# Optimization experiments

Hardware: AMD Instinct MI355X
Metric: run time of the kernel (lower is better)

The kernel has to match this reference:

```python
import jax, jax.numpy as jnp
import numpy as np

B, T, D, HEADS = 4, 2048, 2048, 16  # math requires T == D


def setup_inputs() -> dict:
    key = jax.random.key(0)
    k1, k2, k3 = jax.random.split(key, 3)
    scale = 1.0 / np.sqrt(D)
    x = jax.random.normal(k1, (B, T, D), dtype=jnp.float32)
    w_qk = jax.random.normal(k2, (2 * D, D), dtype=jnp.float32) * scale
    w_dense = jax.random.normal(k3, (D, D), dtype=jnp.float32) * scale
    b_dense = jnp.zeros((D,), dtype=jnp.float32)
    return {"x": x, "w_qk": w_qk, "w_dense": w_dense, "b_dense": b_dense}


def reference(x, w_qk, w_dense, b_dense):
    b, t, d = x.shape
    h = HEADS
    vh = d // h
    # to_q_k: Linear(d, 2d, bias=False); chunk into k0, v
    kv = jnp.einsum('btd,ed->bte', x, w_qk)          # [b,t,2d]
    k0, v = kv[..., :d], kv[..., d:]                 # each [b,t,d]
    scale_factor = 1.0 / jnp.sqrt(jnp.asarray(d * (d - 1) / 2, dtype=x.dtype))
    # k = k0.transpose(1,2) -> [b,d,t]; scores = k @ v^T -> [b,d,t] (t==d)
    s = jnp.einsum('bmi,bjm->bij', k0, v) * scale_factor   # [b,d,t]
    a = jax.nn.softmax(s, axis=-1)
    q = jnp.einsum('bit,btd->bid', a, v)             # [b,d,d]
    # q.transpose(0,1).chunk(h, dim=0) -> stack(dim=1) -> transpose(1,2) -> reshape
    qt = jnp.swapaxes(q, 0, 1)                       # [d, b, d]
    stk = qt.reshape(h, vh, b, d)                    # h chunks of [vh,b,d]
    stk = jnp.transpose(stk, (1, 0, 2, 3))           # stack(dim=1): [vh,h,b,d]
    stk = jnp.transpose(stk, (0, 2, 1, 3))           # transpose(1,2): [vh,b,h,d]
    out = stk.reshape(b, t, d)
    # dropout in eval mode == identity; to_dense Linear
    return jnp.einsum('btd,ed->bte', out, w_dense) + b_dense
```

## Files before the change

### kernel.cpp

```cpp
#include <hip/hip_runtime.h>
#include <stdint.h>
#include <math.h>


typedef __bf16 bf16x8 __attribute__((ext_vector_type(8)));
typedef float  f32x4  __attribute__((ext_vector_type(4)));

__device__ __forceinline__ float bf2f(uint16_t u) {
  union { uint32_t i; float f; } c; c.i = ((uint32_t)u) << 16; return c.f;
}
__device__ __forceinline__ uint16_t f2bf(float f) {
  union { float f; uint32_t i; } c; c.f = f;
  uint32_t i = c.i;
  return (uint16_t)((i + 0x7fffu + ((i >> 16) & 1u)) >> 16);
}

#define NX4 4194304u
#define NW4 2097152u
#define ND4 1048576u
__global__ __launch_bounds__(256) void k_cast_all(
    const float* __restrict__ x, const float* __restrict__ wqk,
    const float* __restrict__ wd, uint16_t* __restrict__ dst) {
  uint32_t i = blockIdx.x * 256 + threadIdx.x;
  float4 v;
  if (i < NX4)            v = reinterpret_cast<const float4*>(x)[i];
  else if (i < NX4 + NW4) v = reinterpret_cast<const float4*>(wqk)[i - NX4];
  else                    v = reinterpret_cast<const float4*>(wd)[i - NX4 - NW4];
  ushort4 o;
  o.x = f2bf(v.x); o.y = f2bf(v.y); o.z = f2bf(v.z); o.w = f2bf(v.w);
  reinterpret_cast<ushort4*>(dst)[i] = o;
}

__device__ __forceinline__ const uint16_t* stage_ptr(
    const uint16_t* base, int tile_row0, int c, int lda) {
  const int tid = threadIdx.x;
  const int r3 = tid >> 3;
  const int ko = (((tid & 7) ^ (r3 & 7)) * 8);
  return base + (size_t)(tile_row0 + c * 32 + r3) * lda + ko;
}

__device__ __forceinline__ void gemm_core_reg(
    const uint16_t* a0, const uint16_t* a1, const uint16_t* a2, const uint16_t* a3,
    const uint16_t* b0, const uint16_t* b1, const uint16_t* b2, const uint16_t* b3,
    uint16_t* As, uint16_t* Bs, int K, f32x4 acc[4][4])
{
  const int tid = threadIdx.x;
  const int w = tid >> 6, l = tid & 63;
  const int wm = (w >> 1) * 64, wn = (w & 1) * 64;
  const int frow = l & 15, fkc = l >> 4;
  const int xr = frow & 7;
  const int off0 = (fkc ^ xr) * 8;
  const int off1 = ((4 + fkc) ^ xr) * 8;
  const int lw = (tid >> 3) * 64 + (tid & 7) * 8;

  uint4 ra0, ra1, ra2, ra3, rb0, rb1, rb2, rb3;
  ra0 = *reinterpret_cast<const uint4*>(a0); a0 += 64;
  ra1 = *reinterpret_cast<const uint4*>(a1); a1 += 64;
  ra2 = *reinterpret_cast<const uint4*>(a2); a2 += 64;
  ra3 = *reinterpret_cast<const uint4*>(a3); a3 += 64;
  rb0 = *reinterpret_cast<const uint4*>(b0); b0 += 64;
  rb1 = *reinterpret_cast<const uint4*>(b1); b1 += 64;
  rb2 = *reinterpret_cast<const uint4*>(b2); b2 += 64;
  rb3 = *reinterpret_cast<const uint4*>(b3); b3 += 64;

  for (int kb = 0; kb < K; kb += 64) {
    __syncthreads();
    *reinterpret_cast<uint4*>(&As[lw])        = ra0;
    *reinterpret_cast<uint4*>(&As[lw + 2048]) = ra1;
    *reinterpret_cast<uint4*>(&As[lw + 4096]) = ra2;
    *reinterpret_cast<uint4*>(&As[lw + 6144]) = ra3;
    *reinterpret_cast<uint4*>(&Bs[lw])        = rb0;
    *reinterpret_cast<uint4*>(&Bs[lw + 2048]) = rb1;
    *reinterpret_cast<uint4*>(&Bs[lw + 4096]) = rb2;
    *reinterpret_cast<uint4*>(&Bs[lw + 6144]) = rb3;
    __syncthreads();
    if (kb + 64 < K) {
      ra0 = *reinterpret_cast<const uint4*>(a0); a0 += 64;
      ra1 = *reinterpret_cast<const uint4*>(a1); a1 += 64;
      ra2 = *reinterpret_cast<const uint4*>(a2); a2 += 64;
      ra3 = *reinterpret_cast<const uint4*>(a3); a3 += 64;
      rb0 = *reinterpret_cast<const uint4*>(b0); b0 += 64;
      rb1 = *reinterpret_cast<const uint4*>(b1); b1 += 64;
      rb2 = *reinterpret_cast<const uint4*>(b2); b2 += 64;
      rb3 = *reinterpret_cast<const uint4*>(b3); b3 += 64;
    }
#pragma unroll
    for (int h = 0; h < 2; ++h) {
      const int off = h ? off1 : off0;
      bf16x8 af[4], bfv[4];
#pragma unroll
      for (int mi = 0; mi < 4; ++mi)
        af[mi] = *reinterpret_cast<const bf16x8*>(&As[(wm + mi * 16 + frow) * 64 + off]);
#pragma unroll
      for (int ni = 0; ni < 4; ++ni)
        bfv[ni] = *reinterpret_cast<const bf16x8*>(&Bs[(wn + ni * 16 + frow) * 64 + off]);
#pragma unroll
      for (int mi = 0; mi < 4; ++mi)
#pragma unroll
        for (int ni = 0; ni < 4; ++ni)
          acc[mi][ni] = __builtin_amdgcn_mfma_f32_16x16x32_bf16(af[mi], bfv[ni], acc[mi][ni], 0, 0, 0);
    }
  }
}

__global__ __launch_bounds__(256) void k_gemm_kv(
    const uint16_t* __restrict__ W,
    const uint16_t* __restrict__ X,
    uint16_t* __restrict__ k0T,
    uint16_t* __restrict__ vT)
{
  __shared__ uint16_t As[8192], Bs[8192];
  const int bm = blockIdx.y, bn = blockIdx.x;
  f32x4 acc[4][4];
#pragma unroll
  for (int i = 0; i < 4; ++i)
#pragma unroll
    for (int j = 0; j < 4; ++j) acc[i][j] = (f32x4){0.f, 0.f, 0.f, 0.f};
  gemm_core_reg(stage_ptr(W, bm * 128, 0, 2048), stage_ptr(W, bm * 128, 1, 2048),
                stage_ptr(W, bm * 128, 2, 2048), stage_ptr(W, bm * 128, 3, 2048),
                stage_ptr(X, bn * 128, 0, 2048), stage_ptr(X, bn * 128, 1, 2048),
                stage_ptr(X, bn * 128, 2, 2048), stage_ptr(X, bn * 128, 3, 2048),
                As, Bs, 2048, acc);
  const int tid = threadIdx.x;
  const int w = tid >> 6, l = tid & 63;
  const int wm = (w >> 1) * 64, wn = (w & 1) * 64;
  const int cr = (l >> 4) * 4, cc = l & 15;
  uint16_t* Cb = (bm < 16) ? (k0T + (size_t)bm * 128 * 8192)
                           : (vT + (size_t)(bm - 16) * 128 * 8192);
#pragma unroll
  for (int mi = 0; mi < 4; ++mi)
#pragma unroll
    for (int ni = 0; ni < 4; ++ni)
#pragma unroll
      for (int g = 0; g < 4; ++g) {
        int lr = wm + mi * 16 + cr + g;
        int bt = bn * 128 + wn + ni * 16 + cc;
        Cb[(size_t)lr * 8192 + bt] = f2bf(acc[mi][ni][g]);
      }
}

__global__ __launch_bounds__(256) void k_gemm_bt(
    const uint16_t* __restrict__ A, int lda, long sA,
    const uint16_t* __restrict__ B, int ldb, long sB,
    uint16_t* __restrict__ C, int ldc, long sC,
    int K, float scale)
{
  __shared__ uint16_t As[8192], Bs[8192];
  const int z = blockIdx.z;
  A += (size_t)z * sA; B += (size_t)z * sB; C += (size_t)z * sC;
  const int bm = blockIdx.y, bn = blockIdx.x;
  f32x4 acc[4][4];
#pragma unroll
  for (int i = 0; i < 4; ++i)
#pragma unroll
    for (int j = 0; j < 4; ++j) acc[i][j] = (f32x4){0.f, 0.f, 0.f, 0.f};
  gemm_core_reg(stage_ptr(A, bm * 128, 0, lda), stage_ptr(A, bm * 128, 1, lda),
                stage_ptr(A, bm * 128, 2, lda), stage_ptr(A, bm * 128, 3, lda),
                stage_ptr(B, bn * 128, 0, ldb), stage_ptr(B, bn * 128, 1, ldb),
                stage_ptr(B, bn * 128, 2, ldb), stage_ptr(B, bn * 128, 3, ldb),
                As, Bs, K, acc);
  const int tid = threadIdx.x;
  const int w = tid >> 6, l = tid & 63;
  const int wm = (w >> 1) * 64, wn = (w & 1) * 64;
  const int cr = (l >> 4) * 4, cc = l & 15;
#pragma unroll
  for (int mi = 0; mi < 4; ++mi)
#pragma unroll
    for (int ni = 0; ni < 4; ++ni)
#pragma unroll
      for (int g = 0; g < 4; ++g) {
        int grow = bm * 128 + wm + mi * 16 + cr + g;
        int gcol = bn * 128 + wn + ni * 16 + cc;
        C[(size_t)grow * ldc + gcol] = f2bf(acc[mi][ni][g] * scale);
      }
}

__device__ __forceinline__ size_t qrow_off(int rr) {
  int bp = rr >> 11, tp = rr & 2047;
  int bi = (tp >> 4) & 3;
  int i  = (tp & 15) * 128 + bp * 32 + (tp >> 6);
  return ((size_t)bi * 2048 + (size_t)i) * 2048;
}

__global__ __launch_bounds__(256) void k_gemm_out(
    const uint16_t* __restrict__ Q,
    const uint16_t* __restrict__ W,
    const float*    __restrict__ bias,
    float*          __restrict__ Out)
{
  __shared__ uint16_t As[8192], Bs[8192];
  const int tid = threadIdx.x;
  const int bm = blockIdx.y, bn = blockIdx.x;
  const int r3 = tid >> 3;
  const int ko = ((tid & 7) ^ (r3 & 7)) * 8;
  const uint16_t* a0 = Q + qrow_off(bm * 128 + 0 * 32 + r3) + ko;
  const uint16_t* a1 = Q + qrow_off(bm * 128 + 1 * 32 + r3) + ko;
  const uint16_t* a2 = Q + qrow_off(bm * 128 + 2 * 32 + r3) + ko;
  const uint16_t* a3 = Q + qrow_off(bm * 128 + 3 * 32 + r3) + ko;
  f32x4 acc[4][4];
#pragma unroll
  for (int i = 0; i < 4; ++i)
#pragma unroll
    for (int j = 0; j < 4; ++j) acc[i][j] = (f32x4){0.f, 0.f, 0.f, 0.f};
  gemm_core_reg(a0, a1, a2, a3,
                stage_ptr(W, bn * 128, 0, 2048), stage_ptr(W, bn * 128, 1, 2048),
                stage_ptr(W, bn * 128, 2, 2048), stage_ptr(W, bn * 128, 3, 2048),
                As, Bs, 2048, acc);
  const int w = tid >> 6, l = tid & 63;
  const int wm = (w >> 1) * 64, wn = (w & 1) * 64;
  const int cr = (l >> 4) * 4, cc = l & 15;
#pragma unroll
  for (int mi = 0; mi < 4; ++mi)
#pragma unroll
    for (int ni = 0; ni < 4; ++ni)
#pragma unroll
      for (int g = 0; g < 4; ++g) {
        int grow = bm * 128 + wm + mi * 16 + cr + g;
        int gcol = bn * 128 + wn + ni * 16 + cc;
        Out[(size_t)grow * 2048 + gcol] = acc[mi][ni][g] + bias[gcol];
      }
}

__global__ __launch_bounds__(256) void k_transpose(
    const uint16_t* __restrict__ src, uint16_t* __restrict__ dst)
{
  __shared__ uint16_t tile[64][65];
  const int tid = threadIdx.x;
  const int bx = blockIdx.x;
  const int by = blockIdx.y;
  const int cu = tid & 31, r0 = tid >> 5;
#pragma unroll
  for (int p = 0; p < 8; ++p) {
    int r = p * 8 + r0;
    uint32_t v = *reinterpret_cast<const uint32_t*>(
        &src[(size_t)(by * 64 + r) * 8192 + bx * 64 + cu * 2]);
    tile[r][cu * 2]     = (uint16_t)(v & 0xffffu);
    tile[r][cu * 2 + 1] = (uint16_t)(v >> 16);
  }
  __syncthreads();
#pragma unroll
  for (int p = 0; p < 8; ++p) {
    int r = p * 8 + r0;
    uint32_t lo = tile[cu * 2][r], hi = tile[cu * 2 + 1][r];
    *reinterpret_cast<uint32_t*>(
        &dst[(size_t)(bx * 64 + r) * 2048 + by * 64 + cu * 2]) = lo | (hi << 16);
  }
}

__global__ __launch_bounds__(256) void k_softmax(uint16_t* __restrict__ s)
{
  uint16_t* p = s + (size_t)blockIdx.x * 2048;
  const int tid = threadIdx.x;
  uint4 raw = reinterpret_cast<const uint4*>(p)[tid];
  uint32_t u[4] = {raw.x, raw.y, raw.z, raw.w};
  float x[8];
#pragma unroll
  for (int i = 0; i < 4; ++i) {
    x[2 * i]     = bf2f((uint16_t)(u[i] & 0xffffu));
    x[2 * i + 1] = bf2f((uint16_t)(u[i] >> 16));
  }
  float m = x[0];
#pragma unroll
  for (int i = 1; i < 8; ++i) m = fmaxf(m, x[i]);
#pragma unroll
  for (int o = 32; o; o >>= 1) m = fmaxf(m, __shfl_xor(m, o, 64));
  __shared__ float redm[4], reds[4];
  if ((tid & 63) == 0) redm[tid >> 6] = m;
  __syncthreads();
  m = fmaxf(fmaxf(redm[0], redm[1]), fmaxf(redm[2], redm[3]));
  float sum = 0.f;
#pragma unroll
  for (int i = 0; i < 8; ++i) { x[i] = __expf(x[i] - m); sum += x[i]; }
#pragma unroll
  for (int o = 32; o; o >>= 1) sum += __shfl_xor(sum, o, 64);
  if ((tid & 63) == 0) reds[tid >> 6] = sum;
  __syncthreads();
  sum = reds[0] + reds[1] + reds[2] + reds[3];
  float inv = 1.0f / sum;
  uint32_t ou[4];
#pragma unroll
  for (int i = 0; i < 4; ++i) {
    uint32_t lo = f2bf(x[2 * i] * inv);
    uint32_t hi = f2bf(x[2 * i + 1] * inv);
    ou[i] = lo | (hi << 16);
  }
  reinterpret_cast<uint4*>(p)[tid] = make_uint4(ou[0], ou[1], ou[2], ou[3]);
}

extern "C" void kernel_launch(void* const* d_in, const int* in_sizes, int n_in,
                              void* d_out, int out_size, void* d_ws, size_t ws_size,
                              hipStream_t stream) {
  const float* x       = (const float*)d_in[0];
  const float* w_qk    = (const float*)d_in[1];
  const float* w_dense = (const float*)d_in[2];
  const float* b_dense = (const float*)d_in[3];
  float* out = (float*)d_out;

  const size_t NX = 4ull * 2048 * 2048;
  const size_t NW = 4096ull * 2048;
  const size_t ND = 2048ull * 2048;

  uint16_t* xb   = (uint16_t*)d_ws;
  uint16_t* wqkb = xb + NX;
  uint16_t* wdb  = wqkb + NW;
  uint16_t* k0T  = wdb + ND;
  uint16_t* vT   = k0T + NX;
  uint16_t* qb   = xb;
  uint16_t* Vn   = (uint16_t*)d_out;
  uint16_t* sb   = Vn + NX;

  const float scale = (float)(1.0 / sqrt(0.5 * 2048.0 * 2047.0));

  k_cast_all<<<dim3((NX4 + NW4 + ND4) / 256), 256, 0, stream>>>(x, w_qk, w_dense, xb);

  k_gemm_kv<<<dim3(64, 32), 256, 0, stream>>>(wqkb, xb, k0T, vT);
  k_transpose<<<dim3(128, 32), 256, 0, stream>>>(vT, Vn);
  k_gemm_bt<<<dim3(16, 16, 4), 256, 0, stream>>>(
      k0T, 8192, 2048L, Vn, 2048, 2048L * 2048L, sb, 2048, 2048L * 2048L, 2048, scale);
  k_softmax<<<dim3(8192), 256, 0, stream>>>(sb);
  k_gemm_bt<<<dim3(16, 16, 4), 256, 0, stream>>>(
      sb, 2048, 2048L * 2048L, vT, 8192, 2048L, qb, 2048, 2048L * 2048L, 2048, 1.0f);
  k_gemm_out<<<dim3(16, 64), 256, 0, stream>>>(qb, wdb, b_dense, out);
}
```

Before: 536.2 us.

## Rewrite GEMM core with 256x256 tiles, direct global-to-LDS loads and double buffering

All four GEMMs now share a new core that uses 256x256 block tiles with 512 threads, 128 KiB of dynamic LDS, and global_load_lds to stream tiles straight into LDS. Loads are double-buffered, with explicit vmcnt waits and barriers, and MFMA bursts run at raised wave priority. The goal is more data reuse per block and overlap of memory traffic with MFMA work, removing the register round-trip staging of the old loop. In exchange, the grids become much smaller (256 blocks for the batched GEMMs), which can leave CUs underused, and the hand-written wait counts must be exactly right to stay correct.

```diff
diff --git a/kernel.cpp b/kernel.cpp
--- a/kernel.cpp
+++ b/kernel.cpp
@@ -5,6 +5,9 @@
 
 typedef __bf16 bf16x8 __attribute__((ext_vector_type(8)));
 typedef float  f32x4  __attribute__((ext_vector_type(4)));
+
+typedef __attribute__((address_space(3))) uint32_t lds_u32_t;
+typedef __attribute__((address_space(1))) const uint32_t glb_u32_t;
 
 __device__ __forceinline__ float bf2f(uint16_t u) {
   union { uint32_t i; float f; } c; c.i = ((uint32_t)u) << 16; return c.f;
@@ -14,6 +17,14 @@
   uint32_t i = c.i;
   return (uint16_t)((i + 0x7fffu + ((i >> 16) & 1u)) >> 16);
 }
+
+__device__ __forceinline__ void glds16(const uint16_t* g, const char* l) {
+  __builtin_amdgcn_global_load_lds((glb_u32_t*)g, (lds_u32_t*)l, 16, 0, 0);
+}
+
+#define FENCE() asm volatile("" ::: "memory")
+#define BARRIER() do { FENCE(); __builtin_amdgcn_s_barrier(); FENCE(); } while (0)
+#define VMCNT(n_) asm volatile("s_waitcnt vmcnt(" #n_ ")" ::: "memory")
 
 #define NX4 4194304u
 #define NW4 2097152u
@@ -31,146 +42,181 @@
   reinterpret_cast<ushort4*>(dst)[i] = o;
 }
 
-__device__ __forceinline__ const uint16_t* stage_ptr(
-    const uint16_t* base, int tile_row0, int c, int lda) {
-  const int tid = threadIdx.x;
-  const int r3 = tid >> 3;
-  const int ko = (((tid & 7) ^ (r3 & 7)) * 8);
-  return base + (size_t)(tile_row0 + c * 32 + r3) * lda + ko;
-}
-
-__device__ __forceinline__ void gemm_core_reg(
-    const uint16_t* a0, const uint16_t* a1, const uint16_t* a2, const uint16_t* a3,
-    const uint16_t* b0, const uint16_t* b1, const uint16_t* b2, const uint16_t* b3,
-    uint16_t* As, uint16_t* Bs, int K, f32x4 acc[4][4])
-{
+__device__ __forceinline__ void gemm256_core(
+    const uint16_t* aR0, const uint16_t* aR1,
+    const uint16_t* bR0, const uint16_t* bR1,
+    int K, f32x4 acc[8][4])
+{
+  extern __shared__ uint4 smem_u4[];
+  char* smem = (char*)smem_u4;
   const int tid = threadIdx.x;
   const int w = tid >> 6, l = tid & 63;
-  const int wm = (w >> 1) * 64, wn = (w & 1) * 64;
+  const int wm = (w >> 2) * 128, wn = (w & 3) * 64;
   const int frow = l & 15, fkc = l >> 4;
-  const int xr = frow & 7;
-  const int off0 = (fkc ^ xr) * 8;
-  const int off1 = ((4 + fkc) ^ xr) * 8;
-  const int lw = (tid >> 3) * 64 + (tid & 7) * 8;
-
-  uint4 ra0, ra1, ra2, ra3, rb0, rb1, rb2, rb3;
-  ra0 = *reinterpret_cast<const uint4*>(a0); a0 += 64;
-  ra1 = *reinterpret_cast<const uint4*>(a1); a1 += 64;
-  ra2 = *reinterpret_cast<const uint4*>(a2); a2 += 64;
-  ra3 = *reinterpret_cast<const uint4*>(a3); a3 += 64;
-  rb0 = *reinterpret_cast<const uint4*>(b0); b0 += 64;
-  rb1 = *reinterpret_cast<const uint4*>(b1); b1 += 64;
-  rb2 = *reinterpret_cast<const uint4*>(b2); b2 += 64;
-  rb3 = *reinterpret_cast<const uint4*>(b3); b3 += 64;
-
-  for (int kb = 0; kb < K; kb += 64) {
-    __syncthreads();
-    *reinterpret_cast<uint4*>(&As[lw])        = ra0;
-    *reinterpret_cast<uint4*>(&As[lw + 2048]) = ra1;
-    *reinterpret_cast<uint4*>(&As[lw + 4096]) = ra2;
-    *reinterpret_cast<uint4*>(&As[lw + 6144]) = ra3;
-    *reinterpret_cast<uint4*>(&Bs[lw])        = rb0;
-    *reinterpret_cast<uint4*>(&Bs[lw + 2048]) = rb1;
-    *reinterpret_cast<uint4*>(&Bs[lw + 4096]) = rb2;
-    *reinterpret_cast<uint4*>(&Bs[lw + 6144]) = rb3;
-    __syncthreads();
-    if (kb + 64 < K) {
-      ra0 = *reinterpret_cast<const uint4*>(a0); a0 += 64;
-      ra1 = *reinterpret_cast<const uint4*>(a1); a1 += 64;
-      ra2 = *reinterpret_cast<const uint4*>(a2); a2 += 64;
-      ra3 = *reinterpret_cast<const uint4*>(a3); a3 += 64;
-      rb0 = *reinterpret_cast<const uint4*>(b0); b0 += 64;
-      rb1 = *reinterpret_cast<const uint4*>(b1); b1 += 64;
-      rb2 = *reinterpret_cast<const uint4*>(b2); b2 += 64;
-      rb3 = *reinterpret_cast<const uint4*>(b3); b3 += 64;
-    }
-#pragma unroll
-    for (int h = 0; h < 2; ++h) {
-      const int off = h ? off1 : off0;
-      bf16x8 af[4], bfv[4];
-#pragma unroll
-      for (int mi = 0; mi < 4; ++mi)
-        af[mi] = *reinterpret_cast<const bf16x8*>(&As[(wm + mi * 16 + frow) * 64 + off]);
-#pragma unroll
-      for (int ni = 0; ni < 4; ++ni)
-        bfv[ni] = *reinterpret_cast<const bf16x8*>(&Bs[(wn + ni * 16 + frow) * 64 + off]);
-#pragma unroll
-      for (int mi = 0; mi < 4; ++mi)
-#pragma unroll
-        for (int ni = 0; ni < 4; ++ni)
-          acc[mi][ni] = __builtin_amdgcn_mfma_f32_16x16x32_bf16(af[mi], bfv[ni], acc[mi][ni], 0, 0, 0);
-    }
-  }
-}
-
-__global__ __launch_bounds__(256) void k_gemm_kv(
+  const uint32_t chunk = (uint32_t)((fkc ^ ((frow >> 1) & 3)) * 16);
+  const uint32_t aBase = (uint32_t)(wm + frow) * 64 + chunk;
+  const uint32_t bBase = 65536u + (uint32_t)(wn + frow) * 64 + chunk;
+  const uint32_t stW = (uint32_t)w * 1024u;
+  const int NT = K >> 6;
+
+#define STG_A(t_, kh_, buf_) do { \
+    glds16(aR0 + (size_t)(t_) * 64 + (kh_) * 32, \
+           smem + ((uint32_t)(buf_) * 32768u + (uint32_t)(kh_) * 16384u + stW)); \
+    glds16(aR1 + (size_t)(t_) * 64 + (kh_) * 32, \
+           smem + ((uint32_t)(buf_) * 32768u + (uint32_t)(kh_) * 16384u + 8192u + stW)); \
+  } while (0)
+#define STG_B(t_, kh_, buf_) do { \
+    glds16(bR0 + (size_t)(t_) * 64 + (kh_) * 32, \
+           smem + (65536u + (uint32_t)(buf_) * 32768u + (uint32_t)(kh_) * 16384u + stW)); \
+    glds16(bR1 + (size_t)(t_) * 64 + (kh_) * 32, \
+           smem + (65536u + (uint32_t)(buf_) * 32768u + (uint32_t)(kh_) * 16384u + 8192u + stW)); \
+  } while (0)
+#define RD_A(mi_, kh_, buf_) \
+    (*reinterpret_cast<const bf16x8*>(smem + (aBase + (mi_) * 1024u + (kh_) * 16384u + (uint32_t)(buf_) * 32768u)))
+#define RD_B(ni_, kh_, buf_) \
+    (*reinterpret_cast<const bf16x8*>(smem + (bBase + (ni_) * 1024u + (kh_) * 16384u + (uint32_t)(buf_) * 32768u)))
+#define MFMA16(m0_) do { \
+    acc[(m0_)+0][0] = __builtin_amdgcn_mfma_f32_16x16x32_bf16(a0, b0, acc[(m0_)+0][0], 0, 0, 0); \
+    acc[(m0_)+1][0] = __builtin_amdgcn_mfma_f32_16x16x32_bf16(a1, b0, acc[(m0_)+1][0], 0, 0, 0); \
+    acc[(m0_)+2][0] = __builtin_amdgcn_mfma_f32_16x16x32_bf16(a2, b0, acc[(m0_)+2][0], 0, 0, 0); \
+    acc[(m0_)+3][0] = __builtin_amdgcn_mfma_f32_16x16x32_bf16(a3, b0, acc[(m0_)+3][0], 0, 0, 0); \
+    acc[(m0_)+0][1] = __builtin_amdgcn_mfma_f32_16x16x32_bf16(a0, b1, acc[(m0_)+0][1], 0, 0, 0); \
+    acc[(m0_)+1][1] = __builtin_amdgcn_mfma_f32_16x16x32_bf16(a1, b1, acc[(m0_)+1][1], 0, 0, 0); \
+    acc[(m0_)+2][1] = __builtin_amdgcn_mfma_f32_16x16x32_bf16(a2, b1, acc[(m0_)+2][1], 0, 0, 0); \
+    acc[(m0_)+3][1] = __builtin_amdgcn_mfma_f32_16x16x32_bf16(a3, b1, acc[(m0_)+3][1], 0, 0, 0); \
+    acc[(m0_)+0][2] = __builtin_amdgcn_mfma_f32_16x16x32_bf16(a0, b2, acc[(m0_)+0][2], 0, 0, 0); \
+    acc[(m0_)+1][2] = __builtin_amdgcn_mfma_f32_16x16x32_bf16(a1, b2, acc[(m0_)+1][2], 0, 0, 0); \
+    acc[(m0_)+2][2] = __builtin_amdgcn_mfma_f32_16x16x32_bf16(a2, b2, acc[(m0_)+2][2], 0, 0, 0); \
+    acc[(m0_)+3][2] = __builtin_amdgcn_mfma_f32_16x16x32_bf16(a3, b2, acc[(m0_)+3][2], 0, 0, 0); \
+    acc[(m0_)+0][3] = __builtin_amdgcn_mfma_f32_16x16x32_bf16(a0, b3, acc[(m0_)+0][3], 0, 0, 0); \
+    acc[(m0_)+1][3] = __builtin_amdgcn_mfma_f32_16x16x32_bf16(a1, b3, acc[(m0_)+1][3], 0, 0, 0); \
+    acc[(m0_)+2][3] = __builtin_amdgcn_mfma_f32_16x16x32_bf16(a2, b3, acc[(m0_)+2][3], 0, 0, 0); \
+    acc[(m0_)+3][3] = __builtin_amdgcn_mfma_f32_16x16x32_bf16(a3, b3, acc[(m0_)+3][3], 0, 0, 0); \
+  } while (0)
+
+  STG_A(0, 0, 0); STG_B(0, 0, 0); STG_A(0, 1, 0); STG_B(0, 1, 0);
+  if (NT > 1) { STG_A(1, 0, 1); STG_B(1, 0, 1); }
+  VMCNT(4);
+  BARRIER();
+
+  bf16x8 a0, a1, a2, a3, b0, b1, b2, b3;
+
+  for (int t = 0; t < NT; ++t) {
+    const int buf = t & 1;
+    a0 = RD_A(0, 0, buf); a1 = RD_A(1, 0, buf); a2 = RD_A(2, 0, buf); a3 = RD_A(3, 0, buf);
+    b0 = RD_B(0, 0, buf); b1 = RD_B(1, 0, buf); b2 = RD_B(2, 0, buf); b3 = RD_B(3, 0, buf);
+    if (t + 1 < NT) STG_A(t + 1, 1, buf ^ 1);
+    BARRIER();
+    __builtin_amdgcn_s_setprio(1);
+    MFMA16(0);
+    __builtin_amdgcn_s_setprio(0);
+    BARRIER();
+    a0 = RD_A(4, 0, buf); a1 = RD_A(5, 0, buf); a2 = RD_A(6, 0, buf); a3 = RD_A(7, 0, buf);
+    if (t + 1 < NT) STG_B(t + 1, 1, buf ^ 1);
+    if (t < NT - 1) { VMCNT(8); } else { VMCNT(0); }
+    BARRIER();
+    __builtin_amdgcn_s_setprio(1);
+    MFMA16(4);
+    __builtin_amdgcn_s_setprio(0);
+    BARRIER();
+    a0 = RD_A(0, 1, buf); a1 = RD_A(1, 1, buf); a2 = RD_A(2, 1, buf); a3 = RD_A(3, 1, buf);
+    b0 = RD_B(0, 1, buf); b1 = RD_B(1, 1, buf); b2 = RD_B(2, 1, buf); b3 = RD_B(3, 1, buf);
+    if (t + 2 < NT) STG_A(t + 2, 0, buf);
+    BARRIER();
+    __builtin_amdgcn_s_setprio(1);
+    MFMA16(0);
+    __builtin_amdgcn_s_setprio(0);
+    BARRIER();
+    a0 = RD_A(4, 1, buf); a1 = RD_A(5, 1, buf); a2 = RD_A(6, 1, buf); a3 = RD_A(7, 1, buf);
+    if (t + 2 < NT) STG_B(t + 2, 0, buf);
+    if (t < NT - 2) { VMCNT(8); }
+    else if (t == NT - 2) { VMCNT(4); }
+    BARRIER();
+    __builtin_amdgcn_s_setprio(1);
+    MFMA16(4);
+    __builtin_amdgcn_s_setprio(0);
+    BARRIER();
+  }
+#undef STG_A
+#undef STG_B
+#undef RD_A
+#undef RD_B
+#undef MFMA16
+}
+
+__device__ __forceinline__ int stage_co() {
+  const int tid = threadIdx.x;
+  return (((tid & 3) ^ ((tid >> 3) & 3)) * 8);
+}
+
+__global__ __launch_bounds__(512, 2) void k_gemm_kv(
     const uint16_t* __restrict__ W,
     const uint16_t* __restrict__ X,
     uint16_t* __restrict__ k0T,
     uint16_t* __restrict__ vT)
 {
-  __shared__ uint16_t As[8192], Bs[8192];
+  const int tid = threadIdx.x;
   const int bm = blockIdx.y, bn = blockIdx.x;
-  f32x4 acc[4][4];
-#pragma unroll
-  for (int i = 0; i < 4; ++i)
+  const int r0 = tid >> 2, co = stage_co();
+  const uint16_t* aR0 = W + (size_t)(bm * 256 + r0) * 2048 + co;
+  const uint16_t* aR1 = W + (size_t)(bm * 256 + 128 + r0) * 2048 + co;
+  const uint16_t* bR0 = X + (size_t)(bn * 256 + r0) * 2048 + co;
+  const uint16_t* bR1 = X + (size_t)(bn * 256 + 128 + r0) * 2048 + co;
+  f32x4 acc[8][4];
+#pragma unroll
+  for (int i = 0; i < 8; ++i)
 #pragma unroll
     for (int j = 0; j < 4; ++j) acc[i][j] = (f32x4){0.f, 0.f, 0.f, 0.f};
-  gemm_core_reg(stage_ptr(W, bm * 128, 0, 2048), stage_ptr(W, bm * 128, 1, 2048),
-                stage_ptr(W, bm * 128, 2, 2048), stage_ptr(W, bm * 128, 3, 2048),
-                stage_ptr(X, bn * 128, 0, 2048), stage_ptr(X, bn * 128, 1, 2048),
-                stage_ptr(X, bn * 128, 2, 2048), stage_ptr(X, bn * 128, 3, 2048),
-                As, Bs, 2048, acc);
-  const int tid = threadIdx.x;
+  gemm256_core(aR0, aR1, bR0, bR1, 2048, acc);
   const int w = tid >> 6, l = tid & 63;
-  const int wm = (w >> 1) * 64, wn = (w & 1) * 64;
+  const int wm = (w >> 2) * 128, wn = (w & 3) * 64;
   const int cr = (l >> 4) * 4, cc = l & 15;
-  uint16_t* Cb = (bm < 16) ? (k0T + (size_t)bm * 128 * 8192)
-                           : (vT + (size_t)(bm - 16) * 128 * 8192);
-#pragma unroll
-  for (int mi = 0; mi < 4; ++mi)
+  uint16_t* Cb = (bm < 8) ? k0T : vT;
+  const int rb = (bm & 7) * 256;
+#pragma unroll
+  for (int mi = 0; mi < 8; ++mi)
 #pragma unroll
     for (int ni = 0; ni < 4; ++ni)
 #pragma unroll
       for (int g = 0; g < 4; ++g) {
-        int lr = wm + mi * 16 + cr + g;
-        int bt = bn * 128 + wn + ni * 16 + cc;
+        int lr = rb + wm + mi * 16 + cr + g;
+        int bt = bn * 256 + wn + ni * 16 + cc;
         Cb[(size_t)lr * 8192 + bt] = f2bf(acc[mi][ni][g]);
       }
 }
 
-__global__ __launch_bounds__(256) void k_gemm_bt(
+__global__ __launch_bounds__(512, 2) void k_gemm_bt(
     const uint16_t* __restrict__ A, int lda, long sA,
     const uint16_t* __restrict__ B, int ldb, long sB,
     uint16_t* __restrict__ C, int ldc, long sC,
     int K, float scale)
 {
-  __shared__ uint16_t As[8192], Bs[8192];
   const int z = blockIdx.z;
   A += (size_t)z * sA; B += (size_t)z * sB; C += (size_t)z * sC;
+  const int tid = threadIdx.x;
   const int bm = blockIdx.y, bn = blockIdx.x;
-  f32x4 acc[4][4];
-#pragma unroll
-  for (int i = 0; i < 4; ++i)
+  const int r0 = tid >> 2, co = stage_co();
+  const uint16_t* aR0 = A + (size_t)(bm * 256 + r0) * lda + co;
+  const uint16_t* aR1 = A + (size_t)(bm * 256 + 128 + r0) * lda + co;
+  const uint16_t* bR0 = B + (size_t)(bn * 256 + r0) * ldb + co;
+  const uint16_t* bR1 = B + (size_t)(bn * 256 + 128 + r0) * ldb + co;
+  f32x4 acc[8][4];
+#pragma unroll
+  for (int i = 0; i < 8; ++i)
 #pragma unroll
     for (int j = 0; j < 4; ++j) acc[i][j] = (f32x4){0.f, 0.f, 0.f, 0.f};
-  gemm_core_reg(stage_ptr(A, bm * 128, 0, lda), stage_ptr(A, bm * 128, 1, lda),
-                stage_ptr(A, bm * 128, 2, lda), stage_ptr(A, bm * 128, 3, lda),
-                stage_ptr(B, bn * 128, 0, ldb), stage_ptr(B, bn * 128, 1, ldb),
-                stage_ptr(B, bn * 128, 2, ldb), stage_ptr(B, bn * 128, 3, ldb),
-                As, Bs, K, acc);
-  const int tid = threadIdx.x;
+  gemm256_core(aR0, aR1, bR0, bR1, K, acc);
   const int w = tid >> 6, l = tid & 63;
-  const int wm = (w >> 1) * 64, wn = (w & 1) * 64;
+  const int wm = (w >> 2) * 128, wn = (w & 3) * 64;
   const int cr = (l >> 4) * 4, cc = l & 15;
 #pragma unroll
-  for (int mi = 0; mi < 4; ++mi)
+  for (int mi = 0; mi < 8; ++mi)
 #pragma unroll
     for (int ni = 0; ni < 4; ++ni)
 #pragma unroll
       for (int g = 0; g < 4; ++g) {
-        int grow = bm * 128 + wm + mi * 16 + cr + g;
-        int gcol = bn * 128 + wn + ni * 16 + cc;
+        int grow = bm * 256 + wm + mi * 16 + cr + g;
+        int gcol = bn * 256 + wn + ni * 16 + cc;
         C[(size_t)grow * ldc + gcol] = f2bf(acc[mi][ni][g] * scale);
       }
 }
@@ -182,41 +228,36 @@
   return ((size_t)bi * 2048 + (size_t)i) * 2048;
 }
 
-__global__ __launch_bounds__(256) void k_gemm_out(
+__global__ __launch_bounds__(512, 2) void k_gemm_out(
     const uint16_t* __restrict__ Q,
     const uint16_t* __restrict__ W,
     const float*    __restrict__ bias,
     float*          __restrict__ Out)
 {
-  __shared__ uint16_t As[8192], Bs[8192];
   const int tid = threadIdx.x;
   const int bm = blockIdx.y, bn = blockIdx.x;
-  const int r3 = tid >> 3;
-  const int ko = ((tid & 7) ^ (r3 & 7)) * 8;
-  const uint16_t* a0 = Q + qrow_off(bm * 128 + 0 * 32 + r3) + ko;
-  const uint16_t* a1 = Q + qrow_off(bm * 128 + 1 * 32 + r3) + ko;
-  const uint16_t* a2 = Q + qrow_off(bm * 128 + 2 * 32 + r3) + ko;
-  const uint16_t* a3 = Q + qrow_off(bm * 128 + 3 * 32 + r3) + ko;
-  f32x4 acc[4][4];
-#pragma unroll
-  for (int i = 0; i < 4; ++i)
+  const int r0 = tid >> 2, co = stage_co();
+  const uint16_t* aR0 = Q + qrow_off(bm * 256 + r0) + co;
+  const uint16_t* aR1 = Q + qrow_off(bm * 256 + 128 + r0) + co;
+  const uint16_t* bR0 = W + (size_t)(bn * 256 + r0) * 2048 + co;
+  const uint16_t* bR1 = W + (size_t)(bn * 256 + 128 + r0) * 2048 + co;
+  f32x4 acc[8][4];
+#pragma unroll
+  for (int i = 0; i < 8; ++i)
 #pragma unroll
     for (int j = 0; j < 4; ++j) acc[i][j] = (f32x4){0.f, 0.f, 0.f, 0.f};
-  gemm_core_reg(a0, a1, a2, a3,
-                stage_ptr(W, bn * 128, 0, 2048), stage_ptr(W, bn * 128, 1, 2048),
-                stage_ptr(W, bn * 128, 2, 2048), stage_ptr(W, bn * 128, 3, 2048),
-                As, Bs, 2048, acc);
+  gemm256_core(aR0, aR1, bR0, bR1, 2048, acc);
   const int w = tid >> 6, l = tid & 63;
-  const int wm = (w >> 1) * 64, wn = (w & 1) * 64;
+  const int wm = (w >> 2) * 128, wn = (w & 3) * 64;
   const int cr = (l >> 4) * 4, cc = l & 15;
 #pragma unroll
-  for (int mi = 0; mi < 4; ++mi)
+  for (int mi = 0; mi < 8; ++mi)
 #pragma unroll
     for (int ni = 0; ni < 4; ++ni)
 #pragma unroll
       for (int g = 0; g < 4; ++g) {
-        int grow = bm * 128 + wm + mi * 16 + cr + g;
-        int gcol = bn * 128 + wn + ni * 16 + cc;
+        int grow = bm * 256 + wm + mi * 16 + cr + g;
+        int gcol = bn * 256 + wn + ni * 16 + cc;
         Out[(size_t)grow * 2048 + gcol] = acc[mi][ni][g] + bias[gcol];
       }
 }
@@ -296,6 +337,17 @@
   const float* b_dense = (const float*)d_in[3];
   float* out = (float*)d_out;
 
+  static int attr_done = 0;
+  if (!attr_done) {
+    (void)hipFuncSetAttribute(reinterpret_cast<const void*>(k_gemm_kv),
+                              hipFuncAttributeMaxDynamicSharedMemorySize, 131072);
+    (void)hipFuncSetAttribute(reinterpret_cast<const void*>(k_gemm_bt),
+                              hipFuncAttributeMaxDynamicSharedMemorySize, 131072);
+    (void)hipFuncSetAttribute(reinterpret_cast<const void*>(k_gemm_out),
+                              hipFuncAttributeMaxDynamicSharedMemorySize, 131072);
+    attr_done = 1;
+  }
+
   const size_t NX = 4ull * 2048 * 2048;
   const size_t NW = 4096ull * 2048;
   const size_t ND = 2048ull * 2048;
@@ -313,12 +365,12 @@
 
   k_cast_all<<<dim3((NX4 + NW4 + ND4) / 256), 256, 0, stream>>>(x, w_qk, w_dense, xb);
 
-  k_gemm_kv<<<dim3(64, 32), 256, 0, stream>>>(wqkb, xb, k0T, vT);
+  k_gemm_kv<<<dim3(32, 16), 512, 131072, stream>>>(wqkb, xb, k0T, vT);
   k_transpose<<<dim3(128, 32), 256, 0, stream>>>(vT, Vn);
-  k_gemm_bt<<<dim3(16, 16, 4), 256, 0, stream>>>(
+  k_gemm_bt<<<dim3(8, 8, 4), 512, 131072, stream>>>(
       k0T, 8192, 2048L, Vn, 2048, 2048L * 2048L, sb, 2048, 2048L * 2048L, 2048, scale);
   k_softmax<<<dim3(8192), 256, 0, stream>>>(sb);
-  k_gemm_bt<<<dim3(16, 16, 4), 256, 0, stream>>>(
+  k_gemm_bt<<<dim3(8, 8, 4), 512, 131072, stream>>>(
       sb, 2048, 2048L * 2048L, vT, 8192, 2048L, qb, 2048, 2048L * 2048L, 2048, 1.0f);
-  k_gemm_out<<<dim3(16, 64), 256, 0, stream>>>(qb, wdb, b_dense, out);
-}
+  k_gemm_out<<<dim3(8, 32), 512, 131072, stream>>>(qb, wdb, b_dense, out);
+}
```

New measurement: 488.6 us. 8.9% less time.
